# Performance work log

Measured on AMD Instinct MI355X. Metric: run time of the kernel, lower is better.

## Reference

```python
import jax, jax.numpy as jnp
import numpy as np

TEMPERATURE = 0.07
COS_EPS = 1e-8          # torch F.cosine_similarity eps
MASK_FILL = -9e15       # value used to mask the diagonal


def setup_inputs() -> dict:
    key = jax.random.key(0)
    k1, k2 = jax.random.split(key)
    B, D = 4096, 256
    z_i = jax.random.normal(k1, (B, D), dtype=jnp.float32)
    z_j = jax.random.normal(k2, (B, D), dtype=jnp.float32)
    return {"z_i": z_i, "z_j": z_j}


def reference(z_i, z_j):
    B = z_i.shape[0]
    z = jnp.concatenate([z_i, z_j], axis=0)                 # [2B, D]
    # cosine similarity = normalized-GEMM (same math as broadcasted version)
    norms = jnp.maximum(jnp.linalg.norm(z, axis=-1, keepdims=True), COS_EPS)
    zn = z / norms                                          # [2B, D]
    sim = zn @ zn.T                                         # [2B, 2B]
    # fused diagonal mask + temperature scale
    diag = jnp.eye(2 * B, dtype=bool)
    logits = jnp.where(diag, MASK_FILL, sim) / TEMPERATURE  # [2B, 2B]
    # positive pair labels: row k pairs with row (k+B) mod 2B
    labels = jnp.concatenate([jnp.arange(B, 2 * B), jnp.arange(0, B)])
    logp = jax.nn.log_softmax(logits, axis=-1)
    loss = -jnp.mean(jnp.take_along_axis(logp, labels[:, None], axis=-1))
    return loss
```

## Files before the change

### kernel.cpp

```cpp
#include <hip/hip_runtime.h>
#include <hip/hip_bf16.h>

#define B_ROWS 4096
#define TWOB   8192
#define DIM    256
#define INV_T  14.285714285714286f

#define BM 128
#define BN 128
#define NSTRIP 8
#define CT_PER_STRIP 8

typedef __bf16 bf16x8 __attribute__((ext_vector_type(8)));
typedef float  f32x4  __attribute__((ext_vector_type(4)));

__global__ __launch_bounds__(256) void normalize_k(const float* __restrict__ zi,
                                                   const float* __restrict__ zj,
                                                   unsigned short* __restrict__ zn,
                                                   float* __restrict__ loss_acc,
                                                   unsigned int* __restrict__ counter) {
    if (blockIdx.x == 0 && threadIdx.x == 0) {
        loss_acc[0] = 0.0f;
        counter[0]  = 0u;
    }
    int wave = threadIdx.x >> 6;
    int lane = threadIdx.x & 63;
    int row  = blockIdx.x * 4 + wave;
    const float* src = (row < B_ROWS) ? (zi + (size_t)row * DIM)
                                      : (zj + (size_t)(row - B_ROWS) * DIM);
    float4 v = reinterpret_cast<const float4*>(src)[lane];
    float ss = v.x * v.x + v.y * v.y + v.z * v.z + v.w * v.w;
#pragma unroll
    for (int off = 32; off >= 1; off >>= 1) ss += __shfl_xor(ss, off);
    float norm = sqrtf(ss);
    norm = fmaxf(norm, 1e-8f);
    float inv = 1.0f / norm;
    ushort4 o;
    o.x = __builtin_bit_cast(unsigned short, __float2bfloat16(v.x * inv));
    o.y = __builtin_bit_cast(unsigned short, __float2bfloat16(v.y * inv));
    o.z = __builtin_bit_cast(unsigned short, __float2bfloat16(v.z * inv));
    o.w = __builtin_bit_cast(unsigned short, __float2bfloat16(v.w * inv));
    reinterpret_cast<ushort4*>(zn)[(size_t)row * 64 + lane] = o;
}

__global__ __launch_bounds__(256) void ntxent_main(const unsigned short* __restrict__ znu,
                                                   float* __restrict__ pos,
                                                   float* __restrict__ strip_sums) {
    const __bf16* zn = (const __bf16*)znu;
    __shared__ __attribute__((aligned(16))) __bf16 As[8][BM * 32];
    __shared__ __attribute__((aligned(16))) __bf16 Bs[2][BN * 32];

    const int tid  = threadIdx.x;
    const int wave = tid >> 6;
    const int lane = tid & 63;
    const int wr = wave >> 1, wc = wave & 1;
    const int quad = lane >> 4, lc = lane & 15;
    const int rt    = blockIdx.x;
    const int strip = blockIdx.y;
    const int row0  = rt * BM;
    const int posTile = (rt + 32) & 63;

    int stg_off[2];
#pragma unroll
    for (int t = 0; t < 2; ++t) {
        int c  = (wave * 2 + t) * 64 + lane;
        int m  = c >> 2;
        int kc = (c & 3) ^ ((m & 3) ^ ((m >> 2) & 3));
        stg_off[t] = m * DIM + kc * 8;
    }

    const int sw    = (lc & 3) ^ ((lc >> 2) & 3);
    const int aBase = (wr * 64 + lc) * 64 + ((quad ^ sw) * 16);
    const int bBase = (wc * 64 + lc) * 64 + ((quad ^ sw) * 16);

#pragma unroll
    for (int kt = 0; kt < 8; ++kt) {
#pragma unroll
        for (int t = 0; t < 2; ++t) {
            const int j = wave * 2 + t;
            const __bf16* ga = zn + row0 * DIM + kt * 32 + stg_off[t];
            __builtin_amdgcn_global_load_lds(
                (const __attribute__((address_space(1))) void*)ga,
                (__attribute__((address_space(3))) void*)((char*)As + kt * 8192 + j * 1024), 16, 0, 0);
        }
    }
    {
        const int col0 = strip * CT_PER_STRIP * BN;
#pragma unroll
        for (int t = 0; t < 2; ++t) {
            const int j = wave * 2 + t;
            const __bf16* gb = zn + col0 * DIM + stg_off[t];
            __builtin_amdgcn_global_load_lds(
                (const __attribute__((address_space(1))) void*)gb,
                (__attribute__((address_space(3))) void*)((char*)Bs + j * 1024), 16, 0, 0);
        }
    }

    f32x4 acc[4][4];
    float rsum[4][4];
#pragma unroll
    for (int mi = 0; mi < 4; ++mi)
#pragma unroll
        for (int r = 0; r < 4; ++r) rsum[mi][r] = 0.0f;

    for (int ct = 0; ct < CT_PER_STRIP; ++ct) {
        const int colTile = strip * CT_PER_STRIP + ct;
        const int col0 = colTile * BN;
#pragma unroll
        for (int mi = 0; mi < 4; ++mi)
#pragma unroll
            for (int ni = 0; ni < 4; ++ni) acc[mi][ni] = f32x4{0.f, 0.f, 0.f, 0.f};

#pragma unroll
        for (int kt = 0; kt < 8; ++kt) {
            __syncthreads();

            {
                const int nct = (kt == 7) ? ct + 1 : ct;
                const int nkt = (kt + 1) & 7;
                if (nct < CT_PER_STRIP) {
                    const int ncol0 = (strip * CT_PER_STRIP + nct) * BN;
#pragma unroll
                    for (int t = 0; t < 2; ++t) {
                        const int j = wave * 2 + t;
                        const __bf16* gb = zn + ncol0 * DIM + nkt * 32 + stg_off[t];
                        __builtin_amdgcn_global_load_lds(
                            (const __attribute__((address_space(1))) void*)gb,
                            (__attribute__((address_space(3))) void*)((char*)Bs + ((kt + 1) & 1) * 8192 + j * 1024),
                            16, 0, 0);
                    }
                }
            }

            bf16x8 af[4], bfr[4];
#pragma unroll
            for (int mi = 0; mi < 4; ++mi)
                af[mi] = *(const bf16x8*)((const char*)As + kt * 8192 + aBase + mi * 1024);
#pragma unroll
            for (int ni = 0; ni < 4; ++ni)
                bfr[ni] = *(const bf16x8*)((const char*)Bs + (kt & 1) * 8192 + bBase + ni * 1024);
#pragma unroll
            for (int mi = 0; mi < 4; ++mi)
#pragma unroll
                for (int ni = 0; ni < 4; ++ni)
                    acc[mi][ni] = __builtin_amdgcn_mfma_f32_16x16x32_bf16(
                        af[mi], bfr[ni], acc[mi][ni], 0, 0, 0);
        }

        const bool special = (colTile == rt) || (colTile == posTile);
#pragma unroll
        for (int mi = 0; mi < 4; ++mi) {
#pragma unroll
            for (int ni = 0; ni < 4; ++ni) {
                f32x4 a = acc[mi][ni];
#pragma unroll
                for (int r = 0; r < 4; ++r) {
                    float logit = a[r] * INV_T;
                    float e = __expf(logit);
                    if (special) {
                        int gr = row0 + wr * 64 + mi * 16 + quad * 4 + r;
                        int gc = col0 + wc * 64 + ni * 16 + lc;
                        if (gc == ((gr + B_ROWS) & (TWOB - 1))) pos[gr] = logit;
                        if (gr == gc) e = 0.0f;
                    }
                    rsum[mi][r] += e;
                }
            }
        }
    }

    __syncthreads();
    float* rowsumL = (float*)As;
#pragma unroll
    for (int mi = 0; mi < 4; ++mi) {
#pragma unroll
        for (int r = 0; r < 4; ++r) {
            float v = rsum[mi][r];
            v += __shfl_xor(v, 1);
            v += __shfl_xor(v, 2);
            v += __shfl_xor(v, 4);
            v += __shfl_xor(v, 8);
            if (lc == 0) rowsumL[wc * BM + wr * 64 + mi * 16 + quad * 4 + r] = v;
        }
    }
    __syncthreads();
    if (tid < BM)
        strip_sums[(size_t)strip * TWOB + row0 + tid] = rowsumL[tid] + rowsumL[BM + tid];
}

__global__ __launch_bounds__(256) void finalize_k(const float* __restrict__ strip_sums,
                                                  const float* __restrict__ pos,
                                                  float* __restrict__ loss_acc,
                                                  unsigned int* __restrict__ counter,
                                                  float* __restrict__ out) {
    __shared__ float wsums[4];
    const int tid = threadIdx.x;
    const int r   = blockIdx.x * 256 + tid;
    float s = 0.0f;
#pragma unroll
    for (int st = 0; st < NSTRIP; ++st) s += strip_sums[(size_t)st * TWOB + r];
    float local = logf(s) - pos[r];
#pragma unroll
    for (int off = 32; off >= 1; off >>= 1) local += __shfl_xor(local, off);
    if ((tid & 63) == 0) wsums[tid >> 6] = local;
    __syncthreads();
    if (tid == 0) {
        float bsum = wsums[0] + wsums[1] + wsums[2] + wsums[3];
        atomicAdd(loss_acc, bsum);
        __threadfence();
        unsigned int done = atomicAdd(counter, 1u);
        if (done == gridDim.x - 1) {
            float total = atomicAdd(loss_acc, 0.0f);
            out[0] = total / (float)TWOB;
        }
    }
}

extern "C" void kernel_launch(void* const* d_in, const int* in_sizes, int n_in,
                              void* d_out, int out_size, void* d_ws, size_t ws_size,
                              hipStream_t stream) {
    const float* zi = (const float*)d_in[0];
    const float* zj = (const float*)d_in[1];
    unsigned short* zn = (unsigned short*)d_ws;
    float* pos        = (float*)((char*)d_ws + (size_t)TWOB * DIM * 2);
    float* strip_sums = pos + TWOB;
    float* loss_acc   = strip_sums + (size_t)NSTRIP * TWOB;
    unsigned int* counter = (unsigned int*)(loss_acc + 1);
    float* out = (float*)d_out;

    normalize_k<<<dim3(TWOB / 4), 256, 0, stream>>>(zi, zj, zn, loss_acc, counter);
    ntxent_main<<<dim3(64, NSTRIP), 256, 0, stream>>>(zn, pos, strip_sums);
    finalize_k<<<dim3(TWOB / 256), 256, 0, stream>>>(strip_sums, pos, loss_acc, counter, out);
}
```

Measured before the change: 107.2 us.

## Fuse normalize, GEMM-softmax and finalize into one persistent kernel with grid barriers

Merges the three kernel launches into a single 512-block kernel. Blocks first normalize rows, then compute the similarity/exp row sums, then finalize the loss, with atomic-counter grid barriers between phases. The control counters are zeroed with a memset. The exponent is also rewritten as exp2f with a prescaled constant. This removes per-launch overhead and tail gaps between kernels. In exchange it depends on all 512 blocks being co-resident, which risks deadlock if they are not, and the spin barriers add their own cost.

```diff
diff --git a/kernel.cpp b/kernel.cpp
--- a/kernel.cpp
+++ b/kernel.cpp
@@ -5,58 +5,71 @@
 #define TWOB   8192
 #define DIM    256
 #define INV_T  14.285714285714286f
+#define EXPSCALE 20.609865074705232f
 
 #define BM 128
 #define BN 128
 #define NSTRIP 8
 #define CT_PER_STRIP 8
+#define NBLK 512
 
 typedef __bf16 bf16x8 __attribute__((ext_vector_type(8)));
 typedef float  f32x4  __attribute__((ext_vector_type(4)));
 
-__global__ __launch_bounds__(256) void normalize_k(const float* __restrict__ zi,
-                                                   const float* __restrict__ zj,
-                                                   unsigned short* __restrict__ zn,
-                                                   float* __restrict__ loss_acc,
-                                                   unsigned int* __restrict__ counter) {
-    if (blockIdx.x == 0 && threadIdx.x == 0) {
-        loss_acc[0] = 0.0f;
-        counter[0]  = 0u;
-    }
-    int wave = threadIdx.x >> 6;
-    int lane = threadIdx.x & 63;
-    int row  = blockIdx.x * 4 + wave;
-    const float* src = (row < B_ROWS) ? (zi + (size_t)row * DIM)
-                                      : (zj + (size_t)(row - B_ROWS) * DIM);
-    float4 v = reinterpret_cast<const float4*>(src)[lane];
-    float ss = v.x * v.x + v.y * v.y + v.z * v.z + v.w * v.w;
-#pragma unroll
-    for (int off = 32; off >= 1; off >>= 1) ss += __shfl_xor(ss, off);
-    float norm = sqrtf(ss);
-    norm = fmaxf(norm, 1e-8f);
-    float inv = 1.0f / norm;
-    ushort4 o;
-    o.x = __builtin_bit_cast(unsigned short, __float2bfloat16(v.x * inv));
-    o.y = __builtin_bit_cast(unsigned short, __float2bfloat16(v.y * inv));
-    o.z = __builtin_bit_cast(unsigned short, __float2bfloat16(v.z * inv));
-    o.w = __builtin_bit_cast(unsigned short, __float2bfloat16(v.w * inv));
-    reinterpret_cast<ushort4*>(zn)[(size_t)row * 64 + lane] = o;
+__device__ __forceinline__ void gbar(unsigned int* cnt) {
+    __syncthreads();
+    if (threadIdx.x == 0) {
+        __threadfence();
+        atomicAdd(cnt, 1u);
+        while (atomicAdd(cnt, 0u) < NBLK) __builtin_amdgcn_s_sleep(8);
+        __threadfence();
+    }
+    __syncthreads();
 }
 
-__global__ __launch_bounds__(256) void ntxent_main(const unsigned short* __restrict__ znu,
-                                                   float* __restrict__ pos,
-                                                   float* __restrict__ strip_sums) {
-    const __bf16* zn = (const __bf16*)znu;
+__global__ __launch_bounds__(256) void ntxent_fused(const float* __restrict__ zi,
+                                                    const float* __restrict__ zj,
+                                                    unsigned short* __restrict__ znu,
+                                                    float* __restrict__ pos,
+                                                    float* __restrict__ strip_sums,
+                                                    unsigned int* __restrict__ ctrl,
+                                                    float* __restrict__ out) {
     __shared__ __attribute__((aligned(16))) __bf16 As[8][BM * 32];
     __shared__ __attribute__((aligned(16))) __bf16 Bs[2][BN * 32];
 
     const int tid  = threadIdx.x;
     const int wave = tid >> 6;
     const int lane = tid & 63;
+    const int bid  = blockIdx.x;
+    float* loss_acc = (float*)(ctrl + 3);
+
+    {
+        const int base = bid * 16 + wave * 4;
+#pragma unroll
+        for (int i = 0; i < 4; ++i) {
+            const int row = base + i;
+            const float* src = (row < B_ROWS) ? (zi + (size_t)row * DIM)
+                                              : (zj + (size_t)(row - B_ROWS) * DIM);
+            float4 v = reinterpret_cast<const float4*>(src)[lane];
+            float ss = v.x * v.x + v.y * v.y + v.z * v.z + v.w * v.w;
+#pragma unroll
+            for (int off = 32; off >= 1; off >>= 1) ss += __shfl_xor(ss, off);
+            float inv = 1.0f / fmaxf(sqrtf(ss), 1e-8f);
+            ushort4 o;
+            o.x = __builtin_bit_cast(unsigned short, __float2bfloat16(v.x * inv));
+            o.y = __builtin_bit_cast(unsigned short, __float2bfloat16(v.y * inv));
+            o.z = __builtin_bit_cast(unsigned short, __float2bfloat16(v.z * inv));
+            o.w = __builtin_bit_cast(unsigned short, __float2bfloat16(v.w * inv));
+            reinterpret_cast<ushort4*>(znu)[(size_t)row * 64 + lane] = o;
+        }
+    }
+    gbar(ctrl + 0);
+
+    const __bf16* zn = (const __bf16*)znu;
     const int wr = wave >> 1, wc = wave & 1;
     const int quad = lane >> 4, lc = lane & 15;
-    const int rt    = blockIdx.x;
-    const int strip = blockIdx.y;
+    const int rt    = bid >> 3;
+    const int strip = bid & 7;
     const int row0  = rt * BM;
     const int posTile = (rt + 32) & 63;
 
@@ -114,7 +127,6 @@
 #pragma unroll
         for (int kt = 0; kt < 8; ++kt) {
             __syncthreads();
-
             {
                 const int nct = (kt == 7) ? ct + 1 : ct;
                 const int nkt = (kt + 1) & 7;
@@ -155,12 +167,11 @@
                 f32x4 a = acc[mi][ni];
 #pragma unroll
                 for (int r = 0; r < 4; ++r) {
-                    float logit = a[r] * INV_T;
-                    float e = __expf(logit);
+                    float e = exp2f(a[r] * EXPSCALE);
                     if (special) {
                         int gr = row0 + wr * 64 + mi * 16 + quad * 4 + r;
                         int gc = col0 + wc * 64 + ni * 16 + lc;
-                        if (gc == ((gr + B_ROWS) & (TWOB - 1))) pos[gr] = logit;
+                        if (gc == ((gr + B_ROWS) & (TWOB - 1))) pos[gr] = a[r] * INV_T;
                         if (gr == gc) e = 0.0f;
                     }
                     rsum[mi][r] += e;
@@ -186,34 +197,27 @@
     __syncthreads();
     if (tid < BM)
         strip_sums[(size_t)strip * TWOB + row0 + tid] = rowsumL[tid] + rowsumL[BM + tid];
-}
-
-__global__ __launch_bounds__(256) void finalize_k(const float* __restrict__ strip_sums,
-                                                  const float* __restrict__ pos,
-                                                  float* __restrict__ loss_acc,
-                                                  unsigned int* __restrict__ counter,
-                                                  float* __restrict__ out) {
-    __shared__ float wsums[4];
-    const int tid = threadIdx.x;
-    const int r   = blockIdx.x * 256 + tid;
-    float s = 0.0f;
-#pragma unroll
-    for (int st = 0; st < NSTRIP; ++st) s += strip_sums[(size_t)st * TWOB + r];
-    float local = logf(s) - pos[r];
-#pragma unroll
-    for (int off = 32; off >= 1; off >>= 1) local += __shfl_xor(local, off);
-    if ((tid & 63) == 0) wsums[tid >> 6] = local;
-    __syncthreads();
-    if (tid == 0) {
-        float bsum = wsums[0] + wsums[1] + wsums[2] + wsums[3];
-        atomicAdd(loss_acc, bsum);
-        __threadfence();
-        unsigned int done = atomicAdd(counter, 1u);
-        if (done == gridDim.x - 1) {
-            float total = atomicAdd(loss_acc, 0.0f);
-            out[0] = total / (float)TWOB;
-        }
-    }
+
+    gbar(ctrl + 1);
+
+    if (wave == 0) {
+        float v = 0.0f;
+        if (lane < 16) {
+            const int r = bid * 16 + lane;
+            float s = 0.0f;
+#pragma unroll
+            for (int st = 0; st < NSTRIP; ++st) s += strip_sums[(size_t)st * TWOB + r];
+            v = logf(s) - pos[r];
+        }
+        v += __shfl_xor(v, 1);
+        v += __shfl_xor(v, 2);
+        v += __shfl_xor(v, 4);
+        v += __shfl_xor(v, 8);
+        if (lane == 0) atomicAdd(loss_acc, v);
+    }
+    gbar(ctrl + 2);
+    if (bid == 0 && tid == 0)
+        out[0] = atomicAdd(loss_acc, 0.0f) / (float)TWOB;
 }
 
 extern "C" void kernel_launch(void* const* d_in, const int* in_sizes, int n_in,
@@ -224,11 +228,9 @@
     unsigned short* zn = (unsigned short*)d_ws;
     float* pos        = (float*)((char*)d_ws + (size_t)TWOB * DIM * 2);
     float* strip_sums = pos + TWOB;
-    float* loss_acc   = strip_sums + (size_t)NSTRIP * TWOB;
-    unsigned int* counter = (unsigned int*)(loss_acc + 1);
+    unsigned int* ctrl = (unsigned int*)(strip_sums + (size_t)NSTRIP * TWOB);
     float* out = (float*)d_out;
 
-    normalize_k<<<dim3(TWOB / 4), 256, 0, stream>>>(zi, zj, zn, loss_acc, counter);
-    ntxent_main<<<dim3(64, NSTRIP), 256, 0, stream>>>(zn, pos, strip_sums);
-    finalize_k<<<dim3(TWOB / 256), 256, 0, stream>>>(strip_sums, pos, loss_acc, counter, out);
+    hipMemsetAsync(ctrl, 0, 4 * sizeof(unsigned int), stream);
+    ntxent_fused<<<dim3(NBLK), 256, 0, stream>>>(zi, zj, zn, pos, strip_sums, ctrl, out);
 }
```

Result: slower. 217.6 us (+102.9%).
